# Performance work log

Hardware: AMD Instinct MI355X
Metric: run time of the kernel (lower is better)

## Reference

```python
import jax, jax.numpy as jnp
import numpy as np

POOLED_SIZES = [11, 8, 6, 4]
Q_POOLED = 2
NUM_HEADS = 2
EPS_ROUND = 1e-3  # module's self.eps used only in aspect-ratio rounding
LN_EPS = 1e-5     # torch nn.LayerNorm default


def _pool_mat(in_size, out_size):
    # PyTorch adaptive_avg_pool1d windows: start=floor(i*in/out), end=ceil((i+1)*in/out)
    M = np.zeros((out_size, in_size), np.float32)
    for i in range(out_size):
        s = (i * in_size) // out_size
        e = -(((-(i + 1)) * in_size) // out_size)
        M[i, s:e] = 1.0 / (e - s)
    return jnp.asarray(M)


def _bilinear_mat(in_size, out_size):
    # PyTorch F.interpolate bilinear, align_corners=False (half-pixel centers, clamped)
    scale = in_size / out_size
    M = np.zeros((out_size, in_size), np.float32)
    for i in range(out_size):
        src = (i + 0.5) * scale - 0.5
        src = min(max(src, 0.0), in_size - 1)
        i0 = int(np.floor(src))
        i1 = min(i0 + 1, in_size - 1)
        w = src - i0
        M[i, i0] += 1.0 - w
        M[i, i1] += w
    return jnp.asarray(M)


def _ln(x, g, b):
    m = jnp.mean(x, axis=-1, keepdims=True)
    v = jnp.mean((x - m) ** 2, axis=-1, keepdims=True)
    return (x - m) * jax.lax.rsqrt(v + LN_EPS) * g + b


def _out_size(p, H, W):
    if W >= H:
        return (p, round(W * p / H + EPS_ROUND))
    return (round(H * p / W + EPS_ROUND), p)


def setup_inputs() -> dict:
    key = jax.random.key(0)
    ks = jax.random.split(key, 12)
    B, C, H, W = 8, 32, 512, 512
    L = len(POOLED_SIZES)
    return {
        "x": jax.random.normal(ks[0], (B, C, H, W), jnp.float32),
        "q_w": jax.random.normal(ks[1], (C, C), jnp.float32) * 0.05,
        "q_b": jax.random.normal(ks[2], (C,), jnp.float32) * 0.01,
        "kv_w": jax.random.normal(ks[3], (C, 2 * C), jnp.float32) * 0.05,
        "kv_b": jax.random.normal(ks[4], (2 * C,), jnp.float32) * 0.01,
        "proj_w": jax.random.normal(ks[5], (C, C), jnp.float32) * 0.05,
        "proj_b": jax.random.normal(ks[6], (C,), jnp.float32) * 0.01,
        "norm_g": jnp.ones((C,), jnp.float32),
        "norm_b": jnp.zeros((C,), jnp.float32),
        "dconv_w": jax.random.normal(ks[7], (L, C, 1, 3, 3), jnp.float32) * 0.05,  # OIHW depthwise, stacked per level
        "dconv_b": jax.random.normal(ks[8], (L, C), jnp.float32) * 0.01,
        "H": 512,
        "W": 512,
    }


def reference(x, q_w, q_b, kv_w, kv_b, proj_w, proj_b, norm_g, norm_b, dconv_w, dconv_b, H, W):
    B, C = x.shape[0], x.shape[1]
    nh = NUM_HEADS
    hd = C // nh
    scale = hd ** (-0.5)

    # ---- query branch: adaptive pool to ~2x2, then linear ----
    qh, qw = _out_size(Q_POOLED, H, W)
    qp = jnp.einsum('ph,bchw,qw->bcpq', _pool_mat(H, qh), x, _pool_mat(W, qw))  # (B,C,qh,qw)
    qt = qp.reshape(B, C, -1).transpose(0, 2, 1)                               # (B,Nq,C)
    q = (qt @ q_w + q_b).reshape(B, -1, nh, hd).transpose(0, 2, 1, 3)          # (B,nh,Nq,hd)

    # ---- KV pyramid: adaptive pool + depthwise conv residual per level ----
    toks = []
    for i, p in enumerate(POOLED_SIZES):
        ph, pw = _out_size(p, H, W)
        pooled = jnp.einsum('ph,bchw,qw->bcpq', _pool_mat(H, ph), x, _pool_mat(W, pw))
        conv = jax.lax.conv_general_dilated(
            pooled, dconv_w[i], window_strides=(1, 1), padding='SAME',
            feature_group_count=C, dimension_numbers=('NCHW', 'OIHW', 'NCHW'))
        conv = conv + dconv_b[i][None, :, None, None]
        toks.append((pooled + conv).reshape(B, C, -1))
    toks = jnp.concatenate(toks, axis=2).transpose(0, 2, 1)  # (B,Nk,C), Nk=237
    toks = _ln(toks, norm_g, norm_b)

    kv = (toks @ kv_w + kv_b).reshape(B, -1, 2, nh, hd).transpose(2, 0, 3, 1, 4)
    k, v = kv[0], kv[1]                                       # (B,nh,Nk,hd)

    # ---- small-scale attention ----
    attn = jax.nn.softmax(jnp.einsum('bhqd,bhkd->bhqk', q, k) * scale, axis=-1)
    o = jnp.einsum('bhqk,bhkd->bhqd', attn, v).transpose(0, 2, 1, 3).reshape(B, -1, C)
    o = o @ proj_w + proj_b                                    # (B,Nq,C)

    # ---- bilinear upsample back to (H,W) ----
    o = o.transpose(0, 2, 1).reshape(B, C, qh, qw)
    out = jnp.einsum('hp,bcpq,wq->bchw', _bilinear_mat(qh, H), o, _bilinear_mat(qw, W))
    return out  # (B,C,H,W), same as module's to_4d output
```

## Files before the change

### kernel.cpp

```cpp
#include <hip/hip_runtime.h>
#include <math.h>

#define BB 8
#define CC 32
#define NTOK 241
#define NKV 237
#define YROWS 31
#define YPAD 520

struct LvlState { int i, s, e; float acc; };

template <int P, int KB>
__device__ __forceinline__ void step_lvl(LvlState& st, float v, int r,
                                         float (*Y)[YPAD], int c) {
  st.acc += v;
  if (r == st.e - 1) {
    Y[KB + st.i][c] = st.acc * (1.0f / (float)(st.e - st.s));
    st.i++;
    int sn = (st.i * 512) / P;
    st.e = ((st.i + 1) * 512 + P - 1) / P;
    st.acc = (sn <= r) ? v : 0.0f;
    st.s = sn;
  }
}

__device__ __forceinline__ void load16(float (&buf)[16],
                                       const float* __restrict__ xp, int r0) {
#pragma unroll
  for (int u = 0; u < 16; ++u) buf[u] = xp[(size_t)(r0 + u) * 512];
}

__device__ __forceinline__ void proc16(float (&buf)[16], int r0, LvlState& sq,
                                       LvlState& s11, LvlState& s8,
                                       LvlState& s6, LvlState& s4,
                                       float (*Y)[YPAD], int c) {
#pragma unroll
  for (int u = 0; u < 16; ++u) {
    float v = buf[u];
    int r = r0 + u;
    step_lvl<2, 0>(sq, v, r, Y, c);
    step_lvl<11, 2>(s11, v, r, Y, c);
    step_lvl<8, 13>(s8, v, r, Y, c);
    step_lvl<6, 21>(s6, v, r, Y, c);
    step_lvl<4, 27>(s4, v, r, Y, c);
  }
}

__global__ __launch_bounds__(512) void pool_kernel(const float* __restrict__ x,
                                                   float* __restrict__ pooled) {
  __shared__ float Ybuf[YROWS][YPAD];

  const int plane = blockIdx.x;
  const int c = threadIdx.x;
  const float* xp = x + (size_t)plane * (512 * 512) + c;

  LvlState sq{0, 0, 256, 0.f};
  LvlState s11{0, 0, 47, 0.f};
  LvlState s8{0, 0, 64, 0.f};
  LvlState s6{0, 0, 86, 0.f};
  LvlState s4{0, 0, 128, 0.f};

  float A[16], B[16], Cb[16];
  load16(A, xp, 0);
  load16(B, xp, 16);
  for (int rb = 0; rb < 480; rb += 48) {
    load16(Cb, xp, rb + 32);
    proc16(A, rb, sq, s11, s8, s6, s4, Ybuf, c);
    load16(A, xp, rb + 48);
    proc16(B, rb + 16, sq, s11, s8, s6, s4, Ybuf, c);
    load16(B, xp, rb + 64);
    proc16(Cb, rb + 32, sq, s11, s8, s6, s4, Ybuf, c);
  }
  proc16(A, 480, sq, s11, s8, s6, s4, Ybuf, c);
  proc16(B, 496, sq, s11, s8, s6, s4, Ybuf, c);
  __syncthreads();

  if (c < NTOK) {
    int k = c, p, kbase, kb;
    if (k < 4)        { p = 2;  kbase = 0;  kb = 0; }
    else if (k < 125) { p = 11; kbase = 2;  kb = 4; }
    else if (k < 189) { p = 8;  kbase = 13; kb = 125; }
    else if (k < 225) { p = 6;  kbase = 21; kb = 189; }
    else              { p = 4;  kbase = 27; kb = 225; }
    int idx = k - kb, i = idx / p, j = idx - i * p;
    int s = (j * 512) / p, e = ((j + 1) * 512 + p - 1) / p;
    const float* row = &Ybuf[kbase + i][0];
    float t0 = 0.f, t1 = 0.f, t2 = 0.f, t3 = 0.f;
    int cc = s;
    for (; cc + 4 <= e; cc += 4) {
      t0 += row[cc]; t1 += row[cc + 1]; t2 += row[cc + 2]; t3 += row[cc + 3];
    }
    for (; cc < e; ++cc) t0 += row[cc];
    pooled[(size_t)plane * NTOK + k] = ((t0 + t1) + (t2 + t3)) / (float)(e - s);
  }
}

__global__ __launch_bounds__(512) void attn_kernel(
    const float* __restrict__ pooled,
    const float* __restrict__ q_w, const float* __restrict__ q_b,
    const float* __restrict__ kv_w, const float* __restrict__ kv_b,
    const float* __restrict__ proj_w, const float* __restrict__ proj_b,
    const float* __restrict__ norm_g, const float* __restrict__ norm_b,
    const float* __restrict__ dconv_w, const float* __restrict__ dconv_b,
    float* __restrict__ o_out) {
  __shared__ float pl[CC * NTOK];
  __shared__ float toks[NKV][33];
  __shared__ float kvls[NKV][65];
  __shared__ float kvw[CC * 64];
  __shared__ float dw[4 * CC * 9];
  __shared__ float dbias[4 * CC];
  __shared__ float qbias[CC], kvb[64], gln[CC], bln[CC];
  __shared__ float qtok[4][CC];
  __shared__ float attno[4][33];

  const int b = blockIdx.x, tid = threadIdx.x;
  const float* plg = pooled + (size_t)b * CC * NTOK;
  for (int i = tid; i < CC * NTOK; i += 512) pl[i] = plg[i];
  for (int i = tid; i < CC * 64; i += 512) kvw[i] = kv_w[i];
  for (int i = tid; i < 4 * CC * 9; i += 512) dw[i] = dconv_w[i];
  if (tid < 4 * CC) dbias[tid] = dconv_b[tid];
  if (tid < CC) { qbias[tid] = q_b[tid]; gln[tid] = norm_g[tid]; bln[tid] = norm_b[tid]; }
  if (tid >= 64 && tid < 128) kvb[tid - 64] = kv_b[tid - 64];
  __syncthreads();

  for (int item = tid; item < NKV * CC; item += 512) {
    int t = item >> 5, c = item & 31;
    int l, p, kb_, tb;
    if (t < 121)      { l = 0; p = 11; kb_ = 4;   tb = 0; }
    else if (t < 185) { l = 1; p = 8;  kb_ = 125; tb = 121; }
    else if (t < 221) { l = 2; p = 6;  kb_ = 189; tb = 185; }
    else              { l = 3; p = 4;  kb_ = 225; tb = 221; }
    int ti = t - tb;
    int i = ti / p, j = ti - i * p;
    const float* plc = pl + c * NTOK + kb_;
    const float* w9 = dw + (l * CC + c) * 9;
    float acc = dbias[l * CC + c];
#pragma unroll
    for (int dy = -1; dy <= 1; ++dy)
#pragma unroll
      for (int dx = -1; dx <= 1; ++dx) {
        int ii = i + dy, jj = j + dx;
        if (ii >= 0 && ii < p && jj >= 0 && jj < p)
          acc += w9[(dy + 1) * 3 + (dx + 1)] * plc[ii * p + jj];
      }
    toks[t][c] = plc[i * p + j] + acc;
  }
  __syncthreads();

  if (tid < NKV) {
    float xv[32]; float m = 0.f;
#pragma unroll
    for (int c = 0; c < 32; ++c) { xv[c] = toks[tid][c]; m += xv[c]; }
    m *= (1.0f / 32.0f);
    float v = 0.f;
#pragma unroll
    for (int c = 0; c < 32; ++c) { float d = xv[c] - m; v += d * d; }
    v *= (1.0f / 32.0f);
    float rs = rsqrtf(v + 1e-5f);
#pragma unroll
    for (int c = 0; c < 32; ++c) toks[tid][c] = (xv[c] - m) * rs * gln[c] + bln[c];
  } else if (tid >= 384) {
    int it = tid - 384;
    int n = it >> 5, u = it & 31;
    float acc = qbias[u];
#pragma unroll
    for (int c = 0; c < 32; ++c) acc += pl[c * NTOK + n] * q_w[c * 32 + u];
    qtok[n][u] = acc * 0.25f;
  }
  __syncthreads();

  for (int item = tid; item < NKV * 64; item += 512) {
    int t = item >> 6, u = item & 63;
    float acc = kvb[u];
#pragma unroll
    for (int c = 0; c < 32; ++c) acc += toks[t][c] * kvw[c * 64 + u];
    kvls[t][u] = acc;
  }
  __syncthreads();

  {
    int wave = tid >> 6, lane = tid & 63;
    int h = wave >> 2, qi = wave & 3;
    float qv[16];
#pragma unroll
    for (int d = 0; d < 16; ++d) qv[d] = qtok[qi][h * 16 + d];
    float sc[4];
#pragma unroll
    for (int m = 0; m < 4; ++m) {
      int t = lane + m * 64;
      float s = -1e30f;
      if (t < NKV) {
        s = 0.f;
#pragma unroll
        for (int d = 0; d < 16; ++d) s += qv[d] * kvls[t][h * 16 + d];
      }
      sc[m] = s;
    }
    float mx = fmaxf(fmaxf(sc[0], sc[1]), fmaxf(sc[2], sc[3]));
#pragma unroll
    for (int d = 1; d < 64; d <<= 1) mx = fmaxf(mx, __shfl_xor(mx, d));
    float pr[4]; float ssum = 0.f;
#pragma unroll
    for (int m = 0; m < 4; ++m) {
      int t = lane + m * 64;
      pr[m] = (t < NKV) ? expf(sc[m] - mx) : 0.0f;
      ssum += pr[m];
    }
#pragma unroll
    for (int d = 1; d < 64; d <<= 1) ssum += __shfl_xor(ssum, d);
    float acc[16];
#pragma unroll
    for (int d = 0; d < 16; ++d) acc[d] = 0.f;
#pragma unroll
    for (int m = 0; m < 4; ++m) {
      int t = lane + m * 64;
      if (t < NKV) {
        float p = pr[m];
#pragma unroll
        for (int d = 0; d < 16; ++d) acc[d] += p * kvls[t][32 + h * 16 + d];
      }
    }
#pragma unroll
    for (int d = 0; d < 16; ++d) {
#pragma unroll
      for (int s = 1; s < 64; s <<= 1) acc[d] += __shfl_xor(acc[d], s);
    }
    if (lane == 0) {
      float inv = 1.0f / ssum;
#pragma unroll
      for (int d = 0; d < 16; ++d) attno[qi][h * 16 + d] = acc[d] * inv;
    }
  }
  __syncthreads();

  if (tid < 128) {
    int n = tid >> 5, u = tid & 31;
    float acc = proj_b[u];
#pragma unroll
    for (int c = 0; c < 32; ++c) acc += attno[n][c] * proj_w[c * 32 + u];
    o_out[((size_t)b * 32 + u) * 4 + n] = acc;
  }
}

__global__ __launch_bounds__(256) void upsample_kernel(const float* __restrict__ o_in,
                                                       float* __restrict__ out) {
  const int plane = blockIdx.x >> 3;
  const int chunk = blockIdx.x & 7;
  const int tid = threadIdx.x;
  const int sub = tid >> 7, col4 = tid & 127;

  const float o00 = o_in[plane * 4 + 0];
  const float o01 = o_in[plane * 4 + 1];
  const float o10 = o_in[plane * 4 + 2];
  const float o11 = o_in[plane * 4 + 3];

  float top[4], bot[4];
#pragma unroll
  for (int k = 0; k < 4; ++k) {
    float c = (float)(4 * col4 + k) + 0.5f;
    float ww = c * (1.0f / 256.0f) - 0.5f;
    ww = fminf(fmaxf(ww, 0.0f), 1.0f);
    top[k] = o00 + ww * (o01 - o00);
    bot[k] = o10 + ww * (o11 - o10);
  }
  float* outp = out + (size_t)plane * (512 * 512);
  const int r0 = chunk * 64;
  for (int i = 0; i < 32; ++i) {
    int r = r0 + 2 * i + sub;
    float wh = ((float)r + 0.5f) * (1.0f / 256.0f) - 0.5f;
    wh = fminf(fmaxf(wh, 0.0f), 1.0f);
    float4 v;
    v.x = top[0] + wh * (bot[0] - top[0]);
    v.y = top[1] + wh * (bot[1] - top[1]);
    v.z = top[2] + wh * (bot[2] - top[2]);
    v.w = top[3] + wh * (bot[3] - top[3]);
    *(float4*)(outp + r * 512 + 4 * col4) = v;
  }
}

extern "C" void kernel_launch(void* const* d_in, const int* in_sizes, int n_in,
                              void* d_out, int out_size, void* d_ws, size_t ws_size,
                              hipStream_t stream) {
  const float* x       = (const float*)d_in[0];
  const float* q_w     = (const float*)d_in[1];
  const float* q_b     = (const float*)d_in[2];
  const float* kv_w    = (const float*)d_in[3];
  const float* kv_b    = (const float*)d_in[4];
  const float* proj_w  = (const float*)d_in[5];
  const float* proj_b  = (const float*)d_in[6];
  const float* norm_g  = (const float*)d_in[7];
  const float* norm_b  = (const float*)d_in[8];
  const float* dconv_w = (const float*)d_in[9];
  const float* dconv_b = (const float*)d_in[10];
  float* out = (float*)d_out;

  float* pooled = (float*)d_ws;
  float* o_ws   = pooled + (size_t)BB * CC * NTOK;

  pool_kernel<<<BB * CC, 512, 0, stream>>>(x, pooled);
  attn_kernel<<<BB, 512, 0, stream>>>(pooled, q_w, q_b, kv_w, kv_b, proj_w,
                                      proj_b, norm_g, norm_b, dconv_w, dconv_b,
                                      o_ws);
  upsample_kernel<<<BB * CC * 8, 256, 0, stream>>>(o_ws, out);
}
```

Baseline: 196.4 us.

## Split pooling over row quarters with atomic merge of boundary windows

Each pooling plane is now processed by four blocks that each stream a 128-row slab. Partial window sums are written directly when the window lies inside the slab, and merged with atomicAdd when it crosses slab boundaries. A memset zeroes the pooled buffer first. This lifts the pool kernel from 256 blocks to 1024 so more CUs stream x concurrently, at the cost of an extra memset launch, some atomics, and non-deterministic summation order.

Measured after the change: 200.0 us. Within noise of the previous version (+1.9%).

```diff
diff --git a/kernel.cpp b/kernel.cpp
--- a/kernel.cpp
+++ b/kernel.cpp
@@ -5,93 +5,129 @@
 #define CC 32
 #define NTOK 241
 #define NKV 237
-#define YROWS 31
-#define YPAD 520
-
-struct LvlState { int i, s, e; float acc; };
-
-template <int P, int KB>
-__device__ __forceinline__ void step_lvl(LvlState& st, float v, int r,
-                                         float (*Y)[YPAD], int c) {
+#define QSPLIT 4
+#define RB 128
+#define NSLOT 10
+#define YPADW 516
+
+struct Lvl { int i; int eh; float acc; };
+
+template <int P>
+__device__ __forceinline__ void lvl_init(Lvl& st, int lo, int hi) {
+  st.i = (lo * P) >> 9;
+  int e = ((st.i + 1) * 512 + P - 1) / P;
+  st.eh = min(e, hi);
+  st.acc = 0.0f;
+}
+
+template <int P, int BASE>
+__device__ __forceinline__ void lvl_step(Lvl& st, float v, int r, int hi,
+                                         float* Y, int c, int& slot) {
   st.acc += v;
-  if (r == st.e - 1) {
-    Y[KB + st.i][c] = st.acc * (1.0f / (float)(st.e - st.s));
+  if (r == st.eh - 1) {
+    Y[(BASE + slot) * YPADW + c] = st.acc;
+    slot++;
     st.i++;
     int sn = (st.i * 512) / P;
-    st.e = ((st.i + 1) * 512 + P - 1) / P;
+    int e = ((st.i + 1) * 512 + P - 1) / P;
+    st.eh = min(e, hi);
     st.acc = (sn <= r) ? v : 0.0f;
-    st.s = sn;
-  }
-}
-
-__device__ __forceinline__ void load16(float (&buf)[16],
-                                       const float* __restrict__ xp, int r0) {
-#pragma unroll
-  for (int u = 0; u < 16; ++u) buf[u] = xp[(size_t)(r0 + u) * 512];
-}
-
-__device__ __forceinline__ void proc16(float (&buf)[16], int r0, LvlState& sq,
-                                       LvlState& s11, LvlState& s8,
-                                       LvlState& s6, LvlState& s4,
-                                       float (*Y)[YPAD], int c) {
-#pragma unroll
-  for (int u = 0; u < 16; ++u) {
-    float v = buf[u];
-    int r = r0 + u;
-    step_lvl<2, 0>(sq, v, r, Y, c);
-    step_lvl<11, 2>(s11, v, r, Y, c);
-    step_lvl<8, 13>(s8, v, r, Y, c);
-    step_lvl<6, 21>(s6, v, r, Y, c);
-    step_lvl<4, 27>(s4, v, r, Y, c);
-  }
+  }
+}
+
+template <int P, int BASE>
+__device__ __forceinline__ void lvl_fin(Lvl& st, int hi, float* Y, int c,
+                                        int& slot) {
+  int sn = (st.i * 512) / P;
+  if (sn < hi) { Y[(BASE + slot) * YPADW + c] = st.acc; slot++; }
 }
 
 __global__ __launch_bounds__(512) void pool_kernel(const float* __restrict__ x,
                                                    float* __restrict__ pooled) {
-  __shared__ float Ybuf[YROWS][YPAD];
-
-  const int plane = blockIdx.x;
+  __shared__ float Ybuf[NSLOT * YPADW];
+
+  const int plane = blockIdx.x >> 2;
+  const int q = blockIdx.x & 3;
+  const int lo = q * RB, hi = lo + RB;
   const int c = threadIdx.x;
   const float* xp = x + (size_t)plane * (512 * 512) + c;
 
-  LvlState sq{0, 0, 256, 0.f};
-  LvlState s11{0, 0, 47, 0.f};
-  LvlState s8{0, 0, 64, 0.f};
-  LvlState s6{0, 0, 86, 0.f};
-  LvlState s4{0, 0, 128, 0.f};
-
-  float A[16], B[16], Cb[16];
-  load16(A, xp, 0);
-  load16(B, xp, 16);
-  for (int rb = 0; rb < 480; rb += 48) {
-    load16(Cb, xp, rb + 32);
-    proc16(A, rb, sq, s11, s8, s6, s4, Ybuf, c);
-    load16(A, xp, rb + 48);
-    proc16(B, rb + 16, sq, s11, s8, s6, s4, Ybuf, c);
-    load16(B, xp, rb + 64);
-    proc16(Cb, rb + 32, sq, s11, s8, s6, s4, Ybuf, c);
-  }
-  proc16(A, 480, sq, s11, s8, s6, s4, Ybuf, c);
-  proc16(B, 496, sq, s11, s8, s6, s4, Ybuf, c);
-  __syncthreads();
-
-  if (c < NTOK) {
-    int k = c, p, kbase, kb;
-    if (k < 4)        { p = 2;  kbase = 0;  kb = 0; }
-    else if (k < 125) { p = 11; kbase = 2;  kb = 4; }
-    else if (k < 189) { p = 8;  kbase = 13; kb = 125; }
-    else if (k < 225) { p = 6;  kbase = 21; kb = 189; }
-    else              { p = 4;  kbase = 27; kb = 225; }
-    int idx = k - kb, i = idx / p, j = idx - i * p;
-    int s = (j * 512) / p, e = ((j + 1) * 512 + p - 1) / p;
-    const float* row = &Ybuf[kbase + i][0];
+  Lvl L2v, L11, L8, L6, L4;
+  lvl_init<2>(L2v, lo, hi);
+  lvl_init<11>(L11, lo, hi);
+  lvl_init<8>(L8, lo, hi);
+  lvl_init<6>(L6, lo, hi);
+  lvl_init<4>(L4, lo, hi);
+  int s2 = 0, s11 = 0, s8 = 0, s6 = 0, s4 = 0;
+
+  float A[8], B[8];
+#pragma unroll
+  for (int u = 0; u < 8; ++u) A[u] = xp[(size_t)(lo + u) * 512];
+
+  for (int cb = 0; cb < RB; cb += 16) {
+#pragma unroll
+    for (int u = 0; u < 8; ++u) B[u] = xp[(size_t)(lo + cb + 8 + u) * 512];
+#pragma unroll
+    for (int u = 0; u < 8; ++u) {
+      float v = A[u]; int r = lo + cb + u;
+      lvl_step<2, 0>(L2v, v, r, hi, Ybuf, c, s2);
+      lvl_step<11, 1>(L11, v, r, hi, Ybuf, c, s11);
+      lvl_step<8, 5>(L8, v, r, hi, Ybuf, c, s8);
+      lvl_step<6, 7>(L6, v, r, hi, Ybuf, c, s6);
+      lvl_step<4, 9>(L4, v, r, hi, Ybuf, c, s4);
+    }
+    if (cb + 16 < RB) {
+#pragma unroll
+      for (int u = 0; u < 8; ++u) A[u] = xp[(size_t)(lo + cb + 16 + u) * 512];
+    }
+#pragma unroll
+    for (int u = 0; u < 8; ++u) {
+      float v = B[u]; int r = lo + cb + 8 + u;
+      lvl_step<2, 0>(L2v, v, r, hi, Ybuf, c, s2);
+      lvl_step<11, 1>(L11, v, r, hi, Ybuf, c, s11);
+      lvl_step<8, 5>(L8, v, r, hi, Ybuf, c, s8);
+      lvl_step<6, 7>(L6, v, r, hi, Ybuf, c, s6);
+      lvl_step<4, 9>(L4, v, r, hi, Ybuf, c, s4);
+    }
+  }
+  lvl_fin<2, 0>(L2v, hi, Ybuf, c, s2);
+  lvl_fin<11, 1>(L11, hi, Ybuf, c, s11);
+  lvl_fin<8, 5>(L8, hi, Ybuf, c, s8);
+  lvl_fin<6, 7>(L6, hi, Ybuf, c, s6);
+  lvl_fin<4, 9>(L4, hi, Ybuf, c, s4);
+  __syncthreads();
+
+  const int Ps[5]  = {2, 11, 8, 6, 4};
+  const int KBs[5] = {0, 4, 125, 189, 225};
+  const int BSs[5] = {0, 1, 5, 7, 9};
+  int ifir[5], cum[6]; cum[0] = 0;
+#pragma unroll
+  for (int l = 0; l < 5; ++l) {
+    int P = Ps[l];
+    ifir[l] = (lo * P) >> 9;
+    int iend = (hi * P + 511) >> 9;
+    cum[l + 1] = cum[l] + (iend - ifir[l]) * P;
+  }
+  if (c < cum[5]) {
+    int l = 0;
+    while (c >= cum[l + 1]) ++l;
+    int P = Ps[l];
+    int rel = c - cum[l];
+    int slot = rel / P, j = rel - slot * P;
+    int i = ifir[l] + slot;
+    int si = (i * 512) / P, ei = ((i + 1) * 512 + P - 1) / P;
+    int sw = (j * 512) / P, ew = ((j + 1) * 512 + P - 1) / P;
+    const float* row = &Ybuf[(BSs[l] + slot) * YPADW];
     float t0 = 0.f, t1 = 0.f, t2 = 0.f, t3 = 0.f;
-    int cc = s;
-    for (; cc + 4 <= e; cc += 4) {
+    int cc = sw;
+    for (; cc + 4 <= ew; cc += 4) {
       t0 += row[cc]; t1 += row[cc + 1]; t2 += row[cc + 2]; t3 += row[cc + 3];
     }
-    for (; cc < e; ++cc) t0 += row[cc];
-    pooled[(size_t)plane * NTOK + k] = ((t0 + t1) + (t2 + t3)) / (float)(e - s);
+    for (; cc < ew; ++cc) t0 += row[cc];
+    float val = ((t0 + t1) + (t2 + t3)) / (float)((ei - si) * (ew - sw));
+    int idx = plane * NTOK + KBs[l] + i * P + j;
+    if (si >= lo && ei <= hi) pooled[idx] = val;
+    else atomicAdd(&pooled[idx], val);
   }
 }
 
@@ -297,7 +333,8 @@
   float* pooled = (float*)d_ws;
   float* o_ws   = pooled + (size_t)BB * CC * NTOK;
 
-  pool_kernel<<<BB * CC, 512, 0, stream>>>(x, pooled);
+  hipMemsetAsync(d_ws, 0, (size_t)BB * CC * NTOK * sizeof(float), stream);
+  pool_kernel<<<BB * CC * QSPLIT, 512, 0, stream>>>(x, pooled);
   attn_kernel<<<BB, 512, 0, stream>>>(pooled, q_w, q_b, kv_w, kv_b, proj_w,
                                       proj_b, norm_g, norm_b, dconv_w, dconv_b,
                                       o_ws);
```

## Fuse pool, attention and upsample into one persistent kernel with grid barriers

Applied to the files above, without the earlier changes.

Replaces the three kernel launches with a single 256-block kernel that pools, synchronises through an atomic grid barrier, runs the per-batch attention in 8 blocks, barriers again, and then upsamples. Shared memory is overlaid by hand so one buffer serves both phases. The aim is to remove launch gaps and inter-kernel drain between the stages. The cost is a spin barrier that depends on all 256 blocks being co-resident, a memset launch for the barrier counters, and a single-pass upsample that now uses 256 blocks instead of 2048.

New measurement: 270.2 us. +37.6%, slower.

```diff
diff --git a/kernel.cpp b/kernel.cpp
--- a/kernel.cpp
+++ b/kernel.cpp
@@ -5,22 +5,54 @@
 #define CC 32
 #define NTOK 241
 #define NKV 237
-#define YROWS 31
-#define YPAD 520
-
-struct LvlState { int i, s, e; float acc; };
-
-template <int P, int KB>
-__device__ __forceinline__ void step_lvl(LvlState& st, float v, int r,
-                                         float (*Y)[YPAD], int c) {
-  st.acc += v;
-  if (r == st.e - 1) {
-    Y[KB + st.i][c] = st.acc * (1.0f / (float)(st.e - st.s));
-    st.i++;
-    int sn = (st.i * 512) / P;
-    st.e = ((st.i + 1) * 512 + P - 1) / P;
-    st.acc = (sn <= r) ? v : 0.0f;
-    st.s = sn;
+#define YPADW 516
+#define NBLK 256
+
+#define S_PL    0
+#define S_TOKS  7712
+#define S_KVLS  15533
+#define S_KVW   30938
+#define S_DW    32986
+#define S_DB    34138
+#define S_QB    34266
+#define S_KVB   34298
+#define S_GLN   34362
+#define S_BLN   34394
+#define S_QTOK  34426
+#define S_ATTNO 34554
+#define SMEM_F  34816
+
+__device__ __forceinline__ void grid_barrier(unsigned* bar) {
+  __syncthreads();
+  if (threadIdx.x == 0) {
+    __threadfence();
+    unsigned old = __hip_atomic_fetch_add(&bar[0], 1u, __ATOMIC_ACQ_REL,
+                                          __HIP_MEMORY_SCOPE_AGENT);
+    if (old == (unsigned)NBLK - 1) {
+      __hip_atomic_store(&bar[1], 1u, __ATOMIC_RELEASE,
+                         __HIP_MEMORY_SCOPE_AGENT);
+    } else {
+      while (__hip_atomic_load(&bar[1], __ATOMIC_ACQUIRE,
+                               __HIP_MEMORY_SCOPE_AGENT) == 0u)
+        __builtin_amdgcn_s_sleep(32);
+    }
+    __threadfence();
+  }
+  __syncthreads();
+}
+
+struct Win { int i, s, e; float acc; };
+
+template <int P, int BASE>
+__device__ __forceinline__ void wstep(Win& w, float v, int r, float* Y, int c) {
+  w.acc += v;
+  if (r == w.e - 1) {
+    Y[(BASE + w.i) * YPADW + c] = w.acc * (1.0f / (float)(w.e - w.s));
+    w.i++;
+    int sn = (w.i * 512) / P;
+    w.acc = (sn <= r) ? v : 0.0f;
+    w.s = sn;
+    w.e = ((w.i + 1) * 512 + P - 1) / P;
   }
 }
 
@@ -30,251 +62,250 @@
   for (int u = 0; u < 16; ++u) buf[u] = xp[(size_t)(r0 + u) * 512];
 }
 
-__device__ __forceinline__ void proc16(float (&buf)[16], int r0, LvlState& sq,
-                                       LvlState& s11, LvlState& s8,
-                                       LvlState& s6, LvlState& s4,
-                                       float (*Y)[YPAD], int c) {
-#pragma unroll
-  for (int u = 0; u < 16; ++u) {
-    float v = buf[u];
-    int r = r0 + u;
-    step_lvl<2, 0>(sq, v, r, Y, c);
-    step_lvl<11, 2>(s11, v, r, Y, c);
-    step_lvl<8, 13>(s8, v, r, Y, c);
-    step_lvl<6, 21>(s6, v, r, Y, c);
-    step_lvl<4, 27>(s4, v, r, Y, c);
-  }
-}
-
-__global__ __launch_bounds__(512) void pool_kernel(const float* __restrict__ x,
-                                                   float* __restrict__ pooled) {
-  __shared__ float Ybuf[YROWS][YPAD];
-
-  const int plane = blockIdx.x;
-  const int c = threadIdx.x;
-  const float* xp = x + (size_t)plane * (512 * 512) + c;
-
-  LvlState sq{0, 0, 256, 0.f};
-  LvlState s11{0, 0, 47, 0.f};
-  LvlState s8{0, 0, 64, 0.f};
-  LvlState s6{0, 0, 86, 0.f};
-  LvlState s4{0, 0, 128, 0.f};
-
-  float A[16], B[16], Cb[16];
-  load16(A, xp, 0);
-  load16(B, xp, 16);
-  for (int rb = 0; rb < 480; rb += 48) {
-    load16(Cb, xp, rb + 32);
-    proc16(A, rb, sq, s11, s8, s6, s4, Ybuf, c);
-    load16(A, xp, rb + 48);
-    proc16(B, rb + 16, sq, s11, s8, s6, s4, Ybuf, c);
-    load16(B, xp, rb + 64);
-    proc16(Cb, rb + 32, sq, s11, s8, s6, s4, Ybuf, c);
-  }
-  proc16(A, 480, sq, s11, s8, s6, s4, Ybuf, c);
-  proc16(B, 496, sq, s11, s8, s6, s4, Ybuf, c);
-  __syncthreads();
-
-  if (c < NTOK) {
-    int k = c, p, kbase, kb;
-    if (k < 4)        { p = 2;  kbase = 0;  kb = 0; }
-    else if (k < 125) { p = 11; kbase = 2;  kb = 4; }
-    else if (k < 189) { p = 8;  kbase = 13; kb = 125; }
-    else if (k < 225) { p = 6;  kbase = 21; kb = 189; }
-    else              { p = 4;  kbase = 27; kb = 225; }
-    int idx = k - kb, i = idx / p, j = idx - i * p;
-    int s = (j * 512) / p, e = ((j + 1) * 512 + p - 1) / p;
-    const float* row = &Ybuf[kbase + i][0];
-    float t0 = 0.f, t1 = 0.f, t2 = 0.f, t3 = 0.f;
-    int cc = s;
-    for (; cc + 4 <= e; cc += 4) {
-      t0 += row[cc]; t1 += row[cc + 1]; t2 += row[cc + 2]; t3 += row[cc + 3];
-    }
-    for (; cc < e; ++cc) t0 += row[cc];
-    pooled[(size_t)plane * NTOK + k] = ((t0 + t1) + (t2 + t3)) / (float)(e - s);
-  }
-}
-
-__global__ __launch_bounds__(512) void attn_kernel(
-    const float* __restrict__ pooled,
+__global__ __launch_bounds__(512) void lrsa_fused(
+    const float* __restrict__ x,
     const float* __restrict__ q_w, const float* __restrict__ q_b,
     const float* __restrict__ kv_w, const float* __restrict__ kv_b,
     const float* __restrict__ proj_w, const float* __restrict__ proj_b,
     const float* __restrict__ norm_g, const float* __restrict__ norm_b,
     const float* __restrict__ dconv_w, const float* __restrict__ dconv_b,
-    float* __restrict__ o_out) {
-  __shared__ float pl[CC * NTOK];
-  __shared__ float toks[NKV][33];
-  __shared__ float kvls[NKV][65];
-  __shared__ float kvw[CC * 64];
-  __shared__ float dw[4 * CC * 9];
-  __shared__ float dbias[4 * CC];
-  __shared__ float qbias[CC], kvb[64], gln[CC], bln[CC];
-  __shared__ float qtok[4][CC];
-  __shared__ float attno[4][33];
-
-  const int b = blockIdx.x, tid = threadIdx.x;
-  const float* plg = pooled + (size_t)b * CC * NTOK;
-  for (int i = tid; i < CC * NTOK; i += 512) pl[i] = plg[i];
-  for (int i = tid; i < CC * 64; i += 512) kvw[i] = kv_w[i];
-  for (int i = tid; i < 4 * CC * 9; i += 512) dw[i] = dconv_w[i];
-  if (tid < 4 * CC) dbias[tid] = dconv_b[tid];
-  if (tid < CC) { qbias[tid] = q_b[tid]; gln[tid] = norm_g[tid]; bln[tid] = norm_b[tid]; }
-  if (tid >= 64 && tid < 128) kvb[tid - 64] = kv_b[tid - 64];
-  __syncthreads();
-
-  for (int item = tid; item < NKV * CC; item += 512) {
-    int t = item >> 5, c = item & 31;
-    int l, p, kb_, tb;
-    if (t < 121)      { l = 0; p = 11; kb_ = 4;   tb = 0; }
-    else if (t < 185) { l = 1; p = 8;  kb_ = 125; tb = 121; }
-    else if (t < 221) { l = 2; p = 6;  kb_ = 189; tb = 185; }
-    else              { l = 3; p = 4;  kb_ = 225; tb = 221; }
-    int ti = t - tb;
-    int i = ti / p, j = ti - i * p;
-    const float* plc = pl + c * NTOK + kb_;
-    const float* w9 = dw + (l * CC + c) * 9;
-    float acc = dbias[l * CC + c];
-#pragma unroll
-    for (int dy = -1; dy <= 1; ++dy)
-#pragma unroll
-      for (int dx = -1; dx <= 1; ++dx) {
-        int ii = i + dy, jj = j + dx;
-        if (ii >= 0 && ii < p && jj >= 0 && jj < p)
-          acc += w9[(dy + 1) * 3 + (dx + 1)] * plc[ii * p + jj];
-      }
-    toks[t][c] = plc[i * p + j] + acc;
-  }
-  __syncthreads();
-
-  if (tid < NKV) {
-    float xv[32]; float m = 0.f;
-#pragma unroll
-    for (int c = 0; c < 32; ++c) { xv[c] = toks[tid][c]; m += xv[c]; }
-    m *= (1.0f / 32.0f);
-    float v = 0.f;
-#pragma unroll
-    for (int c = 0; c < 32; ++c) { float d = xv[c] - m; v += d * d; }
-    v *= (1.0f / 32.0f);
-    float rs = rsqrtf(v + 1e-5f);
-#pragma unroll
-    for (int c = 0; c < 32; ++c) toks[tid][c] = (xv[c] - m) * rs * gln[c] + bln[c];
-  } else if (tid >= 384) {
-    int it = tid - 384;
-    int n = it >> 5, u = it & 31;
-    float acc = qbias[u];
-#pragma unroll
-    for (int c = 0; c < 32; ++c) acc += pl[c * NTOK + n] * q_w[c * 32 + u];
-    qtok[n][u] = acc * 0.25f;
-  }
-  __syncthreads();
-
-  for (int item = tid; item < NKV * 64; item += 512) {
-    int t = item >> 6, u = item & 63;
-    float acc = kvb[u];
-#pragma unroll
-    for (int c = 0; c < 32; ++c) acc += toks[t][c] * kvw[c * 64 + u];
-    kvls[t][u] = acc;
-  }
-  __syncthreads();
+    float* __restrict__ pooled, float* __restrict__ o_ws,
+    unsigned* __restrict__ bars, float* __restrict__ out) {
+  __shared__ float SMEM[SMEM_F];
+
+  const int plane = blockIdx.x;
+  const int tid = threadIdx.x;
 
   {
-    int wave = tid >> 6, lane = tid & 63;
-    int h = wave >> 2, qi = wave & 3;
-    float qv[16];
-#pragma unroll
-    for (int d = 0; d < 16; ++d) qv[d] = qtok[qi][h * 16 + d];
-    float sc[4];
-#pragma unroll
-    for (int m = 0; m < 4; ++m) {
-      int t = lane + m * 64;
-      float s = -1e30f;
-      if (t < NKV) {
-        s = 0.f;
-#pragma unroll
-        for (int d = 0; d < 16; ++d) s += qv[d] * kvls[t][h * 16 + d];
-      }
-      sc[m] = s;
-    }
-    float mx = fmaxf(fmaxf(sc[0], sc[1]), fmaxf(sc[2], sc[3]));
-#pragma unroll
-    for (int d = 1; d < 64; d <<= 1) mx = fmaxf(mx, __shfl_xor(mx, d));
-    float pr[4]; float ssum = 0.f;
-#pragma unroll
-    for (int m = 0; m < 4; ++m) {
-      int t = lane + m * 64;
-      pr[m] = (t < NKV) ? expf(sc[m] - mx) : 0.0f;
-      ssum += pr[m];
-    }
-#pragma unroll
-    for (int d = 1; d < 64; d <<= 1) ssum += __shfl_xor(ssum, d);
-    float acc[16];
-#pragma unroll
-    for (int d = 0; d < 16; ++d) acc[d] = 0.f;
-#pragma unroll
-    for (int m = 0; m < 4; ++m) {
-      int t = lane + m * 64;
-      if (t < NKV) {
-        float p = pr[m];
-#pragma unroll
-        for (int d = 0; d < 16; ++d) acc[d] += p * kvls[t][32 + h * 16 + d];
-      }
-    }
-#pragma unroll
-    for (int d = 0; d < 16; ++d) {
-#pragma unroll
-      for (int s = 1; s < 64; s <<= 1) acc[d] += __shfl_xor(acc[d], s);
-    }
-    if (lane == 0) {
-      float inv = 1.0f / ssum;
-#pragma unroll
-      for (int d = 0; d < 16; ++d) attno[qi][h * 16 + d] = acc[d] * inv;
-    }
-  }
-  __syncthreads();
-
-  if (tid < 128) {
-    int n = tid >> 5, u = tid & 31;
-    float acc = proj_b[u];
-#pragma unroll
-    for (int c = 0; c < 32; ++c) acc += attno[n][c] * proj_w[c * 32 + u];
-    o_out[((size_t)b * 32 + u) * 4 + n] = acc;
-  }
-}
-
-__global__ __launch_bounds__(256) void upsample_kernel(const float* __restrict__ o_in,
-                                                       float* __restrict__ out) {
-  const int plane = blockIdx.x >> 3;
-  const int chunk = blockIdx.x & 7;
-  const int tid = threadIdx.x;
-  const int sub = tid >> 7, col4 = tid & 127;
-
-  const float o00 = o_in[plane * 4 + 0];
-  const float o01 = o_in[plane * 4 + 1];
-  const float o10 = o_in[plane * 4 + 2];
-  const float o11 = o_in[plane * 4 + 3];
-
-  float top[4], bot[4];
-#pragma unroll
-  for (int k = 0; k < 4; ++k) {
-    float c = (float)(4 * col4 + k) + 0.5f;
-    float ww = c * (1.0f / 256.0f) - 0.5f;
-    ww = fminf(fmaxf(ww, 0.0f), 1.0f);
-    top[k] = o00 + ww * (o01 - o00);
-    bot[k] = o10 + ww * (o11 - o10);
-  }
-  float* outp = out + (size_t)plane * (512 * 512);
-  const int r0 = chunk * 64;
-  for (int i = 0; i < 32; ++i) {
-    int r = r0 + 2 * i + sub;
-    float wh = ((float)r + 0.5f) * (1.0f / 256.0f) - 0.5f;
-    wh = fminf(fmaxf(wh, 0.0f), 1.0f);
-    float4 v;
-    v.x = top[0] + wh * (bot[0] - top[0]);
-    v.y = top[1] + wh * (bot[1] - top[1]);
-    v.z = top[2] + wh * (bot[2] - top[2]);
-    v.w = top[3] + wh * (bot[3] - top[3]);
-    *(float4*)(outp + r * 512 + 4 * col4) = v;
+    const int c = tid;
+    const float* xp = x + (size_t)plane * (512 * 512) + c;
+    Win L2v{0, 0, 256, 0.f};
+    Win L11{0, 0, 47, 0.f};
+    Win L8{0, 0, 64, 0.f};
+    Win L6{0, 0, 86, 0.f};
+    Win L4{0, 0, 128, 0.f};
+
+    float A[16], B[16], Cb[16];
+    load16(A, xp, 0);
+    load16(B, xp, 16);
+#define PROC16(BUF, R0)                                                        \
+  _Pragma("unroll") for (int u = 0; u < 16; ++u) {                             \
+    float v = BUF[u]; int r = (R0) + u;                                        \
+    wstep<2, 0>(L2v, v, r, SMEM, c);                                           \
+    wstep<11, 2>(L11, v, r, SMEM, c);                                          \
+    wstep<8, 13>(L8, v, r, SMEM, c);                                           \
+    wstep<6, 21>(L6, v, r, SMEM, c);                                           \
+    wstep<4, 27>(L4, v, r, SMEM, c);                                           \
+  }
+    for (int rb = 0; rb < 480; rb += 48) {
+      load16(Cb, xp, rb + 32);
+      PROC16(A, rb);
+      load16(A, xp, rb + 48);
+      PROC16(B, rb + 16);
+      load16(B, xp, rb + 64);
+      PROC16(Cb, rb + 32);
+    }
+    PROC16(A, 480);
+    PROC16(B, 496);
+#undef PROC16
+    __syncthreads();
+
+    if (c < NTOK) {
+      int k = c, p, kbase, kb;
+      if (k < 4)        { p = 2;  kbase = 0;  kb = 0; }
+      else if (k < 125) { p = 11; kbase = 2;  kb = 4; }
+      else if (k < 189) { p = 8;  kbase = 13; kb = 125; }
+      else if (k < 225) { p = 6;  kbase = 21; kb = 189; }
+      else              { p = 4;  kbase = 27; kb = 225; }
+      int idx = k - kb, i = idx / p, j = idx - i * p;
+      int s = (j * 512) / p, e = ((j + 1) * 512 + p - 1) / p;
+      const float* row = &SMEM[(kbase + i) * YPADW];
+      float t0 = 0.f, t1 = 0.f, t2 = 0.f, t3 = 0.f;
+      int cc = s;
+      for (; cc + 4 <= e; cc += 4) {
+        t0 += row[cc]; t1 += row[cc + 1]; t2 += row[cc + 2]; t3 += row[cc + 3];
+      }
+      for (; cc < e; ++cc) t0 += row[cc];
+      pooled[(size_t)plane * NTOK + k] = ((t0 + t1) + (t2 + t3)) / (float)(e - s);
+    }
+  }
+
+  grid_barrier(bars);
+
+  if (blockIdx.x < BB) {
+    const int b = blockIdx.x;
+    float* pl    = SMEM + S_PL;
+    float* toks  = SMEM + S_TOKS;
+    float* kvls  = SMEM + S_KVLS;
+    float* kvw   = SMEM + S_KVW;
+    float* dw    = SMEM + S_DW;
+    float* dbias = SMEM + S_DB;
+    float* qbias = SMEM + S_QB;
+    float* kvb   = SMEM + S_KVB;
+    float* gln   = SMEM + S_GLN;
+    float* bln   = SMEM + S_BLN;
+    float* qtok  = SMEM + S_QTOK;
+    float* attno = SMEM + S_ATTNO;
+
+    const float* plg = pooled + (size_t)b * CC * NTOK;
+    for (int i = tid; i < CC * NTOK; i += 512) pl[i] = plg[i];
+    for (int i = tid; i < CC * 64; i += 512) kvw[i] = kv_w[i];
+    for (int i = tid; i < 4 * CC * 9; i += 512) dw[i] = dconv_w[i];
+    if (tid < 4 * CC) dbias[tid] = dconv_b[tid];
+    if (tid < CC) { qbias[tid] = q_b[tid]; gln[tid] = norm_g[tid]; bln[tid] = norm_b[tid]; }
+    if (tid >= 64 && tid < 128) kvb[tid - 64] = kv_b[tid - 64];
+    __syncthreads();
+
+    for (int item = tid; item < NKV * CC; item += 512) {
+      int t = item >> 5, c = item & 31;
+      int l, p, kb_, tb;
+      if (t < 121)      { l = 0; p = 11; kb_ = 4;   tb = 0; }
+      else if (t < 185) { l = 1; p = 8;  kb_ = 125; tb = 121; }
+      else if (t < 221) { l = 2; p = 6;  kb_ = 189; tb = 185; }
+      else              { l = 3; p = 4;  kb_ = 225; tb = 221; }
+      int ti = t - tb;
+      int i = ti / p, j = ti - i * p;
+      const float* plc = pl + c * NTOK + kb_;
+      const float* w9 = dw + (l * CC + c) * 9;
+      float acc = dbias[l * CC + c];
+#pragma unroll
+      for (int dy = -1; dy <= 1; ++dy)
+#pragma unroll
+        for (int dx = -1; dx <= 1; ++dx) {
+          int ii = i + dy, jj = j + dx;
+          if (ii >= 0 && ii < p && jj >= 0 && jj < p)
+            acc += w9[(dy + 1) * 3 + (dx + 1)] * plc[ii * p + jj];
+        }
+      toks[t * 33 + c] = plc[i * p + j] + acc;
+    }
+    __syncthreads();
+
+    if (tid < NKV) {
+      float xv[32]; float m = 0.f;
+#pragma unroll
+      for (int c = 0; c < 32; ++c) { xv[c] = toks[tid * 33 + c]; m += xv[c]; }
+      m *= (1.0f / 32.0f);
+      float v = 0.f;
+#pragma unroll
+      for (int c = 0; c < 32; ++c) { float d = xv[c] - m; v += d * d; }
+      v *= (1.0f / 32.0f);
+      float rs = rsqrtf(v + 1e-5f);
+#pragma unroll
+      for (int c = 0; c < 32; ++c)
+        toks[tid * 33 + c] = (xv[c] - m) * rs * gln[c] + bln[c];
+    } else if (tid >= 384) {
+      int it = tid - 384;
+      int n = it >> 5, u = it & 31;
+      float acc = qbias[u];
+#pragma unroll
+      for (int c = 0; c < 32; ++c) acc += pl[c * NTOK + n] * q_w[c * 32 + u];
+      qtok[n * 32 + u] = acc * 0.25f;
+    }
+    __syncthreads();
+
+    for (int item = tid; item < NKV * 64; item += 512) {
+      int t = item >> 6, u = item & 63;
+      float acc = kvb[u];
+#pragma unroll
+      for (int c = 0; c < 32; ++c) acc += toks[t * 33 + c] * kvw[c * 64 + u];
+      kvls[t * 65 + u] = acc;
+    }
+    __syncthreads();
+
+    {
+      int wave = tid >> 6, lane = tid & 63;
+      int h = wave >> 2, qi = wave & 3;
+      float qv[16];
+#pragma unroll
+      for (int d = 0; d < 16; ++d) qv[d] = qtok[qi * 32 + h * 16 + d];
+      float sc[4];
+#pragma unroll
+      for (int m = 0; m < 4; ++m) {
+        int t = lane + m * 64;
+        float s = -1e30f;
+        if (t < NKV) {
+          s = 0.f;
+#pragma unroll
+          for (int d = 0; d < 16; ++d) s += qv[d] * kvls[t * 65 + h * 16 + d];
+        }
+        sc[m] = s;
+      }
+      float mx = fmaxf(fmaxf(sc[0], sc[1]), fmaxf(sc[2], sc[3]));
+#pragma unroll
+      for (int d = 1; d < 64; d <<= 1) mx = fmaxf(mx, __shfl_xor(mx, d));
+      float pr[4]; float ssum = 0.f;
+#pragma unroll
+      for (int m = 0; m < 4; ++m) {
+        int t = lane + m * 64;
+        pr[m] = (t < NKV) ? expf(sc[m] - mx) : 0.0f;
+        ssum += pr[m];
+      }
+#pragma unroll
+      for (int d = 1; d < 64; d <<= 1) ssum += __shfl_xor(ssum, d);
+      float acc[16];
+#pragma unroll
+      for (int d = 0; d < 16; ++d) acc[d] = 0.f;
+#pragma unroll
+      for (int m = 0; m < 4; ++m) {
+        int t = lane + m * 64;
+        if (t < NKV) {
+          float p = pr[m];
+#pragma unroll
+          for (int d = 0; d < 16; ++d) acc[d] += p * kvls[t * 65 + 32 + h * 16 + d];
+        }
+      }
+#pragma unroll
+      for (int d = 0; d < 16; ++d) {
+#pragma unroll
+        for (int s = 1; s < 64; s <<= 1) acc[d] += __shfl_xor(acc[d], s);
+      }
+      if (lane == 0) {
+        float inv = 1.0f / ssum;
+#pragma unroll
+        for (int d = 0; d < 16; ++d) attno[qi * 33 + h * 16 + d] = acc[d] * inv;
+      }
+    }
+    __syncthreads();
+
+    if (tid < 128) {
+      int n = tid >> 5, u = tid & 31;
+      float acc = proj_b[u];
+#pragma unroll
+      for (int c = 0; c < 32; ++c) acc += attno[n * 33 + c] * proj_w[c * 32 + u];
+      o_ws[((size_t)b * 32 + u) * 4 + n] = acc;
+    }
+  }
+
+  grid_barrier(bars + 2);
+
+  {
+    const float o00 = o_ws[plane * 4 + 0];
+    const float o01 = o_ws[plane * 4 + 1];
+    const float o10 = o_ws[plane * 4 + 2];
+    const float o11 = o_ws[plane * 4 + 3];
+    const int sub = tid >> 7, col4 = tid & 127;
+
+    float top[4], bot[4];
+#pragma unroll
+    for (int k = 0; k < 4; ++k) {
+      float cx = (float)(4 * col4 + k) + 0.5f;
+      float ww = cx * (1.0f / 256.0f) - 0.5f;
+      ww = fminf(fmaxf(ww, 0.0f), 1.0f);
+      top[k] = o00 + ww * (o01 - o00);
+      bot[k] = o10 + ww * (o11 - o10);
+    }
+    float* outp = out + (size_t)plane * (512 * 512);
+    for (int i = 0; i < 128; ++i) {
+      int r = 4 * i + sub;
+      float wh = ((float)r + 0.5f) * (1.0f / 256.0f) - 0.5f;
+      wh = fminf(fmaxf(wh, 0.0f), 1.0f);
+      float4 v;
+      v.x = top[0] + wh * (bot[0] - top[0]);
+      v.y = top[1] + wh * (bot[1] - top[1]);
+      v.z = top[2] + wh * (bot[2] - top[2]);
+      v.w = top[3] + wh * (bot[3] - top[3]);
+      *(float4*)(outp + (size_t)r * 512 + 4 * col4) = v;
+    }
   }
 }
 
@@ -294,12 +325,12 @@
   const float* dconv_b = (const float*)d_in[10];
   float* out = (float*)d_out;
 
-  float* pooled = (float*)d_ws;
-  float* o_ws   = pooled + (size_t)BB * CC * NTOK;
-
-  pool_kernel<<<BB * CC, 512, 0, stream>>>(x, pooled);
-  attn_kernel<<<BB, 512, 0, stream>>>(pooled, q_w, q_b, kv_w, kv_b, proj_w,
-                                      proj_b, norm_g, norm_b, dconv_w, dconv_b,
-                                      o_ws);
-  upsample_kernel<<<BB * CC * 8, 256, 0, stream>>>(o_ws, out);
-}
+  unsigned* bars = (unsigned*)d_ws;
+  float* pooled  = (float*)((char*)d_ws + 64);
+  float* o_ws    = pooled + (size_t)BB * CC * NTOK;
+
+  hipMemsetAsync(d_ws, 0, 16, stream);
+  lrsa_fused<<<NBLK, 512, 0, stream>>>(x, q_w, q_b, kv_w, kv_b, proj_w, proj_b,
+                                       norm_g, norm_b, dconv_w, dconv_b,
+                                       pooled, o_ws, bars, out);
+}
```

## Split pooling planes into two row halves with float4 loads staged through LDS

Applied to the files above, without the earlier changes.

Each image plane is now handled by two blocks covering the top and bottom row halves, each owning a subset of the pooling windows. The top half scans 280 rows because windows straddle the midpoint. Rows are read with coalesced float4 loads into a shared-memory band of 8 rows, prefetched one band ahead, instead of scalar strided per-thread loads. The aim is to double the block count for better occupancy and raise memory throughput on the bandwidth-bound pooling pass, at the cost of extra barriers and some duplicated row reads.

Result: slower. 210.4 us (+7.1%).

```diff
diff --git a/kernel.cpp b/kernel.cpp
--- a/kernel.cpp
+++ b/kernel.cpp
@@ -5,93 +5,121 @@
 #define CC 32
 #define NTOK 241
 #define NKV 237
-#define YROWS 31
-#define YPAD 520
-
-struct LvlState { int i, s, e; float acc; };
-
-template <int P, int KB>
-__device__ __forceinline__ void step_lvl(LvlState& st, float v, int r,
-                                         float (*Y)[YPAD], int c) {
-  st.acc += v;
-  if (r == st.e - 1) {
-    Y[KB + st.i][c] = st.acc * (1.0f / (float)(st.e - st.s));
-    st.i++;
-    int sn = (st.i * 512) / P;
-    st.e = ((st.i + 1) * 512 + P - 1) / P;
-    st.acc = (sn <= r) ? v : 0.0f;
-    st.s = sn;
-  }
-}
-
-__device__ __forceinline__ void load16(float (&buf)[16],
-                                       const float* __restrict__ xp, int r0) {
-#pragma unroll
-  for (int u = 0; u < 16; ++u) buf[u] = xp[(size_t)(r0 + u) * 512];
-}
-
-__device__ __forceinline__ void proc16(float (&buf)[16], int r0, LvlState& sq,
-                                       LvlState& s11, LvlState& s8,
-                                       LvlState& s6, LvlState& s4,
-                                       float (*Y)[YPAD], int c) {
-#pragma unroll
-  for (int u = 0; u < 16; ++u) {
-    float v = buf[u];
-    int r = r0 + u;
-    step_lvl<2, 0>(sq, v, r, Y, c);
-    step_lvl<11, 2>(s11, v, r, Y, c);
-    step_lvl<8, 13>(s8, v, r, Y, c);
-    step_lvl<6, 21>(s6, v, r, Y, c);
-    step_lvl<4, 27>(s4, v, r, Y, c);
-  }
+#define YPADW 516
+#define NSLOT 16
+
+struct Win { int idx, s, e, left; float acc; };
+
+template <int P, int SBASE>
+__device__ __forceinline__ void wstep(Win& w, int nown, float v, int r,
+                                      float* __restrict__ Y, int c) {
+  if (w.left > 0) {
+    w.acc += (r >= w.s) ? v : 0.0f;
+    if (r == w.e - 1) {
+      Y[(SBASE + (nown - w.left)) * YPADW + c] = w.acc;
+      w.left--;
+      w.idx++;
+      int sn = (w.idx * 512) / P;
+      w.acc = (sn <= r) ? v : 0.0f;
+      w.s = sn;
+      w.e = ((w.idx + 1) * 512 + P - 1) / P;
+    }
+  }
+}
+
+template <int P>
+__device__ __forceinline__ void winit(Win& w, int i0, int n) {
+  w.idx = i0;
+  w.s = (i0 * 512) / P;
+  w.e = ((i0 + 1) * 512 + P - 1) / P;
+  w.left = n;
+  w.acc = 0.0f;
 }
 
 __global__ __launch_bounds__(512) void pool_kernel(const float* __restrict__ x,
                                                    float* __restrict__ pooled) {
-  __shared__ float Ybuf[YROWS][YPAD];
-
-  const int plane = blockIdx.x;
-  const int c = threadIdx.x;
-  const float* xp = x + (size_t)plane * (512 * 512) + c;
-
-  LvlState sq{0, 0, 256, 0.f};
-  LvlState s11{0, 0, 47, 0.f};
-  LvlState s8{0, 0, 64, 0.f};
-  LvlState s6{0, 0, 86, 0.f};
-  LvlState s4{0, 0, 128, 0.f};
-
-  float A[16], B[16], Cb[16];
-  load16(A, xp, 0);
-  load16(B, xp, 16);
-  for (int rb = 0; rb < 480; rb += 48) {
-    load16(Cb, xp, rb + 32);
-    proc16(A, rb, sq, s11, s8, s6, s4, Ybuf, c);
-    load16(A, xp, rb + 48);
-    proc16(B, rb + 16, sq, s11, s8, s6, s4, Ybuf, c);
-    load16(B, xp, rb + 64);
-    proc16(Cb, rb + 32, sq, s11, s8, s6, s4, Ybuf, c);
-  }
-  proc16(A, 480, sq, s11, s8, s6, s4, Ybuf, c);
-  proc16(B, 496, sq, s11, s8, s6, s4, Ybuf, c);
-  __syncthreads();
-
-  if (c < NTOK) {
-    int k = c, p, kbase, kb;
-    if (k < 4)        { p = 2;  kbase = 0;  kb = 0; }
-    else if (k < 125) { p = 11; kbase = 2;  kb = 4; }
-    else if (k < 189) { p = 8;  kbase = 13; kb = 125; }
-    else if (k < 225) { p = 6;  kbase = 21; kb = 189; }
-    else              { p = 4;  kbase = 27; kb = 225; }
-    int idx = k - kb, i = idx / p, j = idx - i * p;
-    int s = (j * 512) / p, e = ((j + 1) * 512 + p - 1) / p;
-    const float* row = &Ybuf[kbase + i][0];
+  __shared__ float sh[8 * 512];
+  __shared__ float Ybuf[NSLOT * YPADW];
+
+  const int plane = blockIdx.x >> 1;
+  const int q = blockIdx.x & 1;
+  const int tid = threadIdx.x;
+  const int c = tid;
+
+  const int lo = q ? 256 : 0;
+  const int nb = q ? 32 : 35;
+  int i0_2, n_2, i0_11, n_11, i0_8, n_8, i0_6, n_6, i0_4, n_4;
+  if (q == 0) {
+    i0_2 = 0; n_2 = 1; i0_11 = 0; n_11 = 6; i0_8 = 0; n_8 = 4;
+    i0_6 = 0; n_6 = 3; i0_4 = 0; n_4 = 2;
+  } else {
+    i0_2 = 1; n_2 = 1; i0_11 = 6; n_11 = 5; i0_8 = 4; n_8 = 4;
+    i0_6 = 3; n_6 = 3; i0_4 = 2; n_4 = 2;
+  }
+
+  Win W2, W11, W8, W6, W4;
+  winit<2>(W2, i0_2, n_2);
+  winit<11>(W11, i0_11, n_11);
+  winit<8>(W8, i0_8, n_8);
+  winit<6>(W6, i0_6, n_6);
+  winit<4>(W4, i0_4, n_4);
+
+  const float* xp = x + (size_t)plane * (512 * 512);
+  const int row0 = tid >> 7;
+  const int cg = (tid & 127) * 4;
+
+  float4 r0 = *(const float4*)(xp + (size_t)(lo + row0) * 512 + cg);
+  float4 r1 = *(const float4*)(xp + (size_t)(lo + row0 + 4) * 512 + cg);
+
+  for (int band = 0; band < nb; ++band) {
+    *(float4*)(sh + row0 * 512 + cg) = r0;
+    *(float4*)(sh + (row0 + 4) * 512 + cg) = r1;
+    __syncthreads();
+    if (band + 1 < nb) {
+      int rb = lo + (band + 1) * 8;
+      r0 = *(const float4*)(xp + (size_t)(rb + row0) * 512 + cg);
+      r1 = *(const float4*)(xp + (size_t)(rb + row0 + 4) * 512 + cg);
+    }
+#pragma unroll
+    for (int rr = 0; rr < 8; ++rr) {
+      float v = sh[rr * 512 + c];
+      int r = lo + band * 8 + rr;
+      wstep<2, 0>(W2, n_2, v, r, Ybuf, c);
+      wstep<11, 1>(W11, n_11, v, r, Ybuf, c);
+      wstep<8, 7>(W8, n_8, v, r, Ybuf, c);
+      wstep<6, 11>(W6, n_6, v, r, Ybuf, c);
+      wstep<4, 14>(W4, n_4, v, r, Ybuf, c);
+    }
+    __syncthreads();
+  }
+
+  const int Ps[5]  = {2, 11, 8, 6, 4};
+  const int KBs[5] = {0, 4, 125, 189, 225};
+  const int SBs[5] = {0, 1, 7, 11, 14};
+  const int i0s[5] = {i0_2, i0_11, i0_8, i0_6, i0_4};
+  const int ns[5]  = {n_2, n_11, n_8, n_6, n_4};
+  int cum[6]; cum[0] = 0;
+#pragma unroll
+  for (int l = 0; l < 5; ++l) cum[l + 1] = cum[l] + ns[l] * Ps[l];
+
+  if (tid < cum[5]) {
+    int l = 0;
+    while (tid >= cum[l + 1]) ++l;
+    int P = Ps[l];
+    int rel = tid - cum[l];
+    int li = rel / P, j = rel - li * P;
+    int i = i0s[l] + li;
+    int s = (i * 512) / P, e = ((i + 1) * 512 + P - 1) / P;
+    int sw = (j * 512) / P, ew = ((j + 1) * 512 + P - 1) / P;
+    const float* row = &Ybuf[(SBs[l] + li) * YPADW];
     float t0 = 0.f, t1 = 0.f, t2 = 0.f, t3 = 0.f;
-    int cc = s;
-    for (; cc + 4 <= e; cc += 4) {
+    int cc = sw;
+    for (; cc + 4 <= ew; cc += 4) {
       t0 += row[cc]; t1 += row[cc + 1]; t2 += row[cc + 2]; t3 += row[cc + 3];
     }
-    for (; cc < e; ++cc) t0 += row[cc];
-    pooled[(size_t)plane * NTOK + k] = ((t0 + t1) + (t2 + t3)) / (float)(e - s);
+    for (; cc < ew; ++cc) t0 += row[cc];
+    float val = ((t0 + t1) + (t2 + t3)) / (float)((e - s) * (ew - sw));
+    pooled[(size_t)plane * NTOK + KBs[l] + i * P + j] = val;
   }
 }
 
@@ -297,7 +325,7 @@
   float* pooled = (float*)d_ws;
   float* o_ws   = pooled + (size_t)BB * CC * NTOK;
 
-  pool_kernel<<<BB * CC, 512, 0, stream>>>(x, pooled);
+  pool_kernel<<<BB * CC * 2, 512, 0, stream>>>(x, pooled);
   attn_kernel<<<BB, 512, 0, stream>>>(pooled, q_w, q_b, kv_w, kv_b, proj_w,
                                       proj_b, norm_g, norm_b, dconv_w, dconv_b,
                                       o_ws);
```
